# Kernel optimization log

Measured on AMD Instinct MI355X. Metric: run time of the kernel, lower is better.

Reference implementation:

```python
import jax, jax.numpy as jnp
import numpy as np


def setup_inputs() -> dict:
    key = jax.random.key(0)
    ks = jax.random.split(key, 8)
    b, l, d_model = 2, 2048, 1024
    d_inner, d_state, dt_rank, d_conv = 2048, 16, 64, 4
    g = lambda k, shape, s: jax.random.normal(k, shape, jnp.float32) * s
    A = jnp.broadcast_to(jnp.arange(1, d_state + 1, dtype=jnp.float32), (d_inner, d_state))
    return {
        "x": g(ks[0], (b, l, d_model), 1.0),
        "W_in": g(ks[1], (d_model, 2 * d_inner), 0.02),
        "W_conv": g(ks[2], (d_inner, 1, d_conv), 0.1),
        "b_conv": g(ks[3], (d_inner,), 0.1),
        "W_x": g(ks[4], (d_inner, dt_rank + 2 * d_state), 0.02),
        "W_dt": g(ks[5], (dt_rank, d_inner), 0.02),
        "b_dt": g(ks[6], (d_inner,), 0.1),
        "A_log": jnp.log(A),
        "D": jnp.ones((d_inner,), jnp.float32),
        "W_out": g(ks[7], (d_inner, d_model), 0.02),
    }


def _selective_scan(x, delta, A, B, C, D):
    # x, delta: (b, l, d); A: (d, n); B, C: (b, l, n); D: (d,)
    b, l, d = x.shape
    n = A.shape[1]

    def step(h, inp):
        dt, Bt, Ct, xt = inp  # (b,d), (b,n), (b,n), (b,d)
        dA = jnp.exp(dt[:, :, None] * A)                     # (b,d,n)
        h = dA * h + (dt * xt)[:, :, None] * Bt[:, None, :]  # (b,d,n)
        y = jnp.einsum('bdn,bn->bd', h, Ct)
        return h, y

    h0 = jnp.zeros((b, d, n), x.dtype)
    xs = (jnp.swapaxes(delta, 0, 1), jnp.swapaxes(B, 0, 1),
          jnp.swapaxes(C, 0, 1), jnp.swapaxes(x, 0, 1))
    _, ys = jax.lax.scan(step, h0, xs)   # ys: (l, b, d)
    return jnp.swapaxes(ys, 0, 1) + D * x


def _mamba(x, W_in, W_conv, b_conv, W_x, W_dt, b_dt, A_log, D, W_out):
    b, l, _ = x.shape
    d_inner = W_conv.shape[0]
    d_conv = W_conv.shape[2]
    dt_rank = W_dt.shape[0]
    n = A_log.shape[1]

    xr = x @ W_in                                   # (b,l,2*d_inner)
    xin, res = xr[..., :d_inner], xr[..., d_inner:]

    # depthwise causal conv1d (left pad d_conv-1 == torch pad both + trim to l)
    xc = jnp.swapaxes(xin, 1, 2)                    # (b,d_inner,l)
    xc = jax.lax.conv_general_dilated(
        xc, W_conv, window_strides=(1,), padding=[(d_conv - 1, 0)],
        feature_group_count=d_inner,
        dimension_numbers=('NCH', 'OIH', 'NCH')) + b_conv[None, :, None]
    xs = jax.nn.silu(jnp.swapaxes(xc, 1, 2))        # (b,l,d_inner)

    x_dbl = xs @ W_x                                # (b,l,dt_rank+2n)
    delta = jax.nn.softplus(x_dbl[..., :dt_rank] @ W_dt + b_dt)
    Bm = x_dbl[..., dt_rank:dt_rank + n]
    Cm = x_dbl[..., dt_rank + n:]
    A = -jnp.exp(A_log)

    y = _selective_scan(xs, delta, A, Bm, Cm, D)
    y = y * jax.nn.silu(res)
    return y @ W_out


def reference(x, W_in, W_conv, b_conv, W_x, W_dt, b_dt, A_log, D, W_out):
    return _mamba(x, W_in, W_conv, b_conv, W_x, W_dt, b_dt, A_log, D, W_out)
```

## Files before the change

kernel.cpp:

```cpp
#include <hip/hip_runtime.h>


typedef unsigned short ushort_t;
using short8 = __attribute__((ext_vector_type(8))) short;
using f32x4  = __attribute__((ext_vector_type(4))) float;
using gptr_t = const __attribute__((address_space(1))) unsigned short*;
using sptr_t = __attribute__((address_space(3))) unsigned short*;

#define NC 64
#define CL 32

__device__ inline ushort_t f2bf(float v) {
    unsigned u = __float_as_uint(v);
    unsigned r = (u + 0x7fff + ((u >> 16) & 1)) >> 16;
    return (ushort_t)r;
}
__device__ inline float bf2f(ushort_t h) { return __uint_as_float(((unsigned)h) << 16); }
__device__ inline void split2(float v, ushort_t& h, ushort_t& l) {
    h = f2bf(v);
    l = f2bf(v - bf2f(h));
}


__global__ void split_plain4(const float* __restrict__ in, ushort_t* __restrict__ h,
                             ushort_t* __restrict__ l, int n4) {
    int i = blockIdx.x * blockDim.x + threadIdx.x;
    if (i >= n4) return;
    float4 v = ((const float4*)in)[i];
    ushort4 hh, ll;
    split2(v.x, hh.x, ll.x); split2(v.y, hh.y, ll.y);
    split2(v.z, hh.z, ll.z); split2(v.w, hh.w, ll.w);
    ((ushort4*)h)[i] = hh;
    ((ushort4*)l)[i] = ll;
}

__global__ __launch_bounds__(256) void split_transpose(
    const float* __restrict__ W, ushort_t* __restrict__ Th, ushort_t* __restrict__ Tl,
    int K, int N) {
    __shared__ float tile[32][33];
    int n0 = blockIdx.x * 32, k0 = blockIdx.y * 32;
    int tx = threadIdx.x & 31, ty = threadIdx.x >> 5;
    #pragma unroll
    for (int j = 0; j < 4; ++j) {
        int k = ty + j * 8;
        tile[k][tx] = (n0 + tx < N) ? W[(size_t)(k0 + k) * N + n0 + tx] : 0.f;
    }
    __syncthreads();
    #pragma unroll
    for (int j = 0; j < 4; ++j) {
        int nrow = ty + j * 8;
        float v = tile[tx][nrow];
        ushort_t h, l;
        split2(v, h, l);
        size_t o = (size_t)(n0 + nrow) * K + k0 + tx;
        Th[o] = h; Tl[o] = l;
    }
}

__global__ __launch_bounds__(256) void gemm_mfma3(
    const ushort_t* __restrict__ Ah, const ushort_t* __restrict__ Al,
    const ushort_t* __restrict__ Bh, const ushort_t* __restrict__ Bl,
    float* __restrict__ C, int M, int N, int K) {
    __shared__ ushort_t sAh[4096], sAl[4096], sBh[4096], sBl[4096];
    const int tid  = threadIdx.x;
    const int wid  = tid >> 6;
    const int lane = tid & 63;
    const int bm = blockIdx.y * 128;
    const int bn = blockIdx.x * 128;
    const int wr = wid >> 1, wc = wid & 1;

    f32x4 acc[4][4];
    #pragma unroll
    for (int i = 0; i < 4; ++i)
        #pragma unroll
        for (int j = 0; j < 4; ++j) acc[i][j] = (f32x4){0.f, 0.f, 0.f, 0.f};

    for (int k0 = 0; k0 < K; k0 += 32) {
        #pragma unroll
        for (int issue = 0; issue < 2; ++issue) {
            const int off = wid * 2048 + issue * 1024 + lane * 16;
            const int row = off >> 6;
            const int ce  = (off & 63) >> 1;
            const size_t ga = (size_t)(bm + row) * K + k0 + ce;
            const size_t gb = (size_t)(bn + row) * K + k0 + ce;
            const int lo = (wid * 2048 + issue * 1024) >> 1;
            __builtin_amdgcn_global_load_lds((gptr_t)(Ah + ga), (sptr_t)&sAh[lo], 16, 0, 0);
            __builtin_amdgcn_global_load_lds((gptr_t)(Al + ga), (sptr_t)&sAl[lo], 16, 0, 0);
            __builtin_amdgcn_global_load_lds((gptr_t)(Bh + gb), (sptr_t)&sBh[lo], 16, 0, 0);
            __builtin_amdgcn_global_load_lds((gptr_t)(Bl + gb), (sptr_t)&sBl[lo], 16, 0, 0);
        }
        __syncthreads();

        const int fr = lane & 15;
        const int kb = (lane >> 4) * 8;
        short8 ah[4], al[4], bh[4], bl[4];
        #pragma unroll
        for (int i = 0; i < 4; ++i) {
            const int ra = (wr * 64 + i * 16 + fr) * 32 + kb;
            ah[i] = *(const short8*)&sAh[ra];
            al[i] = *(const short8*)&sAl[ra];
            const int rb = (wc * 64 + i * 16 + fr) * 32 + kb;
            bh[i] = *(const short8*)&sBh[rb];
            bl[i] = *(const short8*)&sBl[rb];
        }
        #pragma unroll
        for (int i = 0; i < 4; ++i)
            #pragma unroll
            for (int j = 0; j < 4; ++j) {
                acc[i][j] = __builtin_amdgcn_mfma_f32_16x16x32_bf16(ah[i], bh[j], acc[i][j], 0, 0, 0);
                acc[i][j] = __builtin_amdgcn_mfma_f32_16x16x32_bf16(ah[i], bl[j], acc[i][j], 0, 0, 0);
                acc[i][j] = __builtin_amdgcn_mfma_f32_16x16x32_bf16(al[i], bh[j], acc[i][j], 0, 0, 0);
            }
        __syncthreads();
    }

    #pragma unroll
    for (int i = 0; i < 4; ++i) {
        int row = bm + wr * 64 + i * 16 + (lane >> 4) * 4;
        #pragma unroll
        for (int j = 0; j < 4; ++j) {
            int col = bn + wc * 64 + j * 16 + (lane & 15);
            float* cp = C + (size_t)row * N + col;
            #pragma unroll
            for (int r = 0; r < 4; ++r) cp[(size_t)r * N] = acc[i][j][r];
        }
    }
}

__global__ __launch_bounds__(256) void gemm_mfma3_sk(
    const ushort_t* __restrict__ Ah, const ushort_t* __restrict__ Al,
    const ushort_t* __restrict__ Bh, const ushort_t* __restrict__ Bl,
    float* __restrict__ partial, int K) {
    __shared__ ushort_t sAh[4096], sAl[4096], sBh[4096], sBl[4096];
    const int tid  = threadIdx.x;
    const int wid  = tid >> 6;
    const int lane = tid & 63;
    const int kslice = blockIdx.x;
    const int bm = blockIdx.y * 128;
    const int wr = wid >> 1, wc = wid & 1;
    const int kbeg = kslice * 256;

    f32x4 acc[4][4];
    #pragma unroll
    for (int i = 0; i < 4; ++i)
        #pragma unroll
        for (int j = 0; j < 4; ++j) acc[i][j] = (f32x4){0.f, 0.f, 0.f, 0.f};

    for (int k0 = kbeg; k0 < kbeg + 256; k0 += 32) {
        #pragma unroll
        for (int issue = 0; issue < 2; ++issue) {
            const int off = wid * 2048 + issue * 1024 + lane * 16;
            const int row = off >> 6;
            const int ce  = (off & 63) >> 1;
            const size_t ga = (size_t)(bm + row) * K + k0 + ce;
            const size_t gb = (size_t)row * K + k0 + ce;
            const int lo = (wid * 2048 + issue * 1024) >> 1;
            __builtin_amdgcn_global_load_lds((gptr_t)(Ah + ga), (sptr_t)&sAh[lo], 16, 0, 0);
            __builtin_amdgcn_global_load_lds((gptr_t)(Al + ga), (sptr_t)&sAl[lo], 16, 0, 0);
            __builtin_amdgcn_global_load_lds((gptr_t)(Bh + gb), (sptr_t)&sBh[lo], 16, 0, 0);
            __builtin_amdgcn_global_load_lds((gptr_t)(Bl + gb), (sptr_t)&sBl[lo], 16, 0, 0);
        }
        __syncthreads();

        const int fr = lane & 15;
        const int kb = (lane >> 4) * 8;
        short8 ah[4], al[4], bh[4], bl[4];
        #pragma unroll
        for (int i = 0; i < 4; ++i) {
            const int ra = (wr * 64 + i * 16 + fr) * 32 + kb;
            ah[i] = *(const short8*)&sAh[ra];
            al[i] = *(const short8*)&sAl[ra];
            const int rb = (wc * 64 + i * 16 + fr) * 32 + kb;
            bh[i] = *(const short8*)&sBh[rb];
            bl[i] = *(const short8*)&sBl[rb];
        }
        #pragma unroll
        for (int i = 0; i < 4; ++i)
            #pragma unroll
            for (int j = 0; j < 4; ++j) {
                acc[i][j] = __builtin_amdgcn_mfma_f32_16x16x32_bf16(ah[i], bh[j], acc[i][j], 0, 0, 0);
                acc[i][j] = __builtin_amdgcn_mfma_f32_16x16x32_bf16(ah[i], bl[j], acc[i][j], 0, 0, 0);
                acc[i][j] = __builtin_amdgcn_mfma_f32_16x16x32_bf16(al[i], bh[j], acc[i][j], 0, 0, 0);
            }
        __syncthreads();
    }

    float* Cp = partial + (size_t)kslice * 4096 * 128;
    #pragma unroll
    for (int i = 0; i < 4; ++i) {
        int row = bm + wr * 64 + i * 16 + (lane >> 4) * 4;
        #pragma unroll
        for (int j = 0; j < 4; ++j) {
            int col = wc * 64 + j * 16 + (lane & 15);
            float* cp = Cp + (size_t)row * 128 + col;
            #pragma unroll
            for (int r = 0; r < 4; ++r) cp[(size_t)r * 128] = acc[i][j][r];
        }
    }
}

__global__ void reduce8(const float4* __restrict__ p, float4* __restrict__ outp) {
    int i = blockIdx.x * 256 + threadIdx.x;
    float4 s = p[i];
    #pragma unroll
    for (int k = 1; k < 8; ++k) {
        float4 v = p[i + k * 131072];
        s.x += v.x; s.y += v.y; s.z += v.z; s.w += v.w;
    }
    outp[i] = s;
}

#define BM 64
#define BN 64
#define BKK 16
__global__ __launch_bounds__(256) void gemm_f32(
    const float* __restrict__ A, const float* __restrict__ B, float* __restrict__ C,
    int M, int N, int K, int lda, int ldb, int ldc,
    const float* __restrict__ bias, int epi) {
    __shared__ float As[BKK][BM];
    __shared__ float Bs[BKK][BN];
    const int bm = blockIdx.y * BM;
    const int bn = blockIdx.x * BN;
    const int tid = threadIdx.x;
    const int tx = tid & 15;
    const int ty = tid >> 4;
    const int a_row = tid >> 2;
    const int a_col = (tid & 3) * 4;
    const int b_row = tid >> 4;
    const int b_col = (tid & 15) * 4;
    const bool fullN = (bn + BN <= N);

    float acc[4][4] = {};
    for (int k0 = 0; k0 < K; k0 += BKK) {
        {
            const float* ap = A + (size_t)(bm + a_row) * lda + (k0 + a_col);
            float4 av = *(const float4*)ap;
            As[a_col + 0][a_row] = av.x; As[a_col + 1][a_row] = av.y;
            As[a_col + 2][a_row] = av.z; As[a_col + 3][a_row] = av.w;
        }
        {
            const float* bp = B + (size_t)(k0 + b_row) * ldb + (bn + b_col);
            float4 bv;
            if (fullN) bv = *(const float4*)bp;
            else {
                bv.x = bv.y = bv.z = bv.w = 0.f;
                int rem = N - (bn + b_col);
                if (rem > 0) bv.x = bp[0];
                if (rem > 1) bv.y = bp[1];
                if (rem > 2) bv.z = bp[2];
                if (rem > 3) bv.w = bp[3];
            }
            Bs[b_row][b_col + 0] = bv.x; Bs[b_row][b_col + 1] = bv.y;
            Bs[b_row][b_col + 2] = bv.z; Bs[b_row][b_col + 3] = bv.w;
        }
        __syncthreads();
        #pragma unroll
        for (int k = 0; k < BKK; ++k) {
            float a[4], b[4];
            #pragma unroll
            for (int i = 0; i < 4; ++i) a[i] = As[k][ty * 4 + i];
            #pragma unroll
            for (int j = 0; j < 4; ++j) b[j] = Bs[k][tx * 4 + j];
            #pragma unroll
            for (int i = 0; i < 4; ++i)
                #pragma unroll
                for (int j = 0; j < 4; ++j)
                    acc[i][j] = fmaf(a[i], b[j], acc[i][j]);
        }
        __syncthreads();
    }
    #pragma unroll
    for (int i = 0; i < 4; ++i) {
        int r = bm + ty * 4 + i;
        #pragma unroll
        for (int j = 0; j < 4; ++j) {
            int col = bn + tx * 4 + j;
            if (col < N) {
                float v = acc[i][j];
                if (epi == 1) {
                    v += bias[col];
                    v = (v > 20.f) ? v : log1pf(__expf(v));
                }
                C[(size_t)r * ldc + col] = v;
            }
        }
    }
}

__global__ void conv_silu_k(const float* __restrict__ xr, const float* __restrict__ Wc,
                            const float* __restrict__ bc, float* __restrict__ xs,
                            ushort_t* __restrict__ xsh, ushort_t* __restrict__ xsl,
                            int total) {
    for (int idx = blockIdx.x * blockDim.x + threadIdx.x; idx < total;
         idx += gridDim.x * blockDim.x) {
        int d = idx & 2047;
        int l = (idx >> 11) & 2047;
        int b = idx >> 22;
        float acc = bc[d];
        const float* wp = Wc + d * 4;
        #pragma unroll
        for (int k = 0; k < 4; ++k) {
            int ll = l - 3 + k;
            if (ll >= 0)
                acc = fmaf(xr[((size_t)(b * 2048 + ll) << 12) + d], wp[k], acc);
        }
        float v = acc / (1.f + __expf(-acc));
        xs[idx] = v;
        ushort_t h, lo;
        split2(v, h, lo);
        xsh[idx] = h;
        xsl[idx] = lo;
    }
}


__global__ __launch_bounds__(256) void scan_p1(
    const float* __restrict__ delta, const float* __restrict__ xs,
    const float* __restrict__ xdbl, const float* __restrict__ A_log,
    float* __restrict__ S, float* __restrict__ sumdt) {
    const int u = blockIdx.x * 256 + threadIdx.x;
    const int chunk = u >> 12;
    const int c = u & 4095;
    const int b = c >> 11, d = c & 2047;

    float a[16];
    #pragma unroll
    for (int i = 0; i < 4; ++i) {
        float4 v = ((const float4*)(A_log + d * 16))[i];
        a[4 * i + 0] = -__expf(v.x); a[4 * i + 1] = -__expf(v.y);
        a[4 * i + 2] = -__expf(v.z); a[4 * i + 3] = -__expf(v.w);
    }
    float h[16];
    #pragma unroll
    for (int n = 0; n < 16; ++n) h[n] = 0.f;
    float sdt = 0.f;

    const size_t row0 = (size_t)b * 2048 + (size_t)chunk * CL;
    const float4* xd4 = (const float4*)xdbl;
    #pragma unroll 2
    for (int t = 0; t < CL; ++t) {
        const size_t row = row0 + t;
        float dt = delta[row * 2048 + d];
        float xv = xs[row * 2048 + d];
        float4 Bv[4];
        #pragma unroll
        for (int i = 0; i < 4; ++i) Bv[i] = xd4[row * 32 + 16 + i];
        const float* Bf = (const float*)Bv;
        sdt += dt;
        float du = dt * xv;
        #pragma unroll
        for (int n = 0; n < 16; ++n) {
            float dA = __expf(dt * a[n]);
            h[n] = fmaf(dA, h[n], du * Bf[n]);
        }
    }
    float4* S4 = (float4*)(S + ((size_t)chunk * 4096 + c) * 16);
    #pragma unroll
    for (int i = 0; i < 4; ++i)
        S4[i] = make_float4(h[4 * i + 0], h[4 * i + 1], h[4 * i + 2], h[4 * i + 3]);
    sumdt[chunk * 4096 + c] = sdt;
}

__global__ __launch_bounds__(256) void scan_p2(
    float* __restrict__ S, const float* __restrict__ sumdt,
    const float* __restrict__ A_log) {
    const int idx = blockIdx.x * blockDim.x + threadIdx.x;
    const int n = idx & 15;
    const int c = (idx >> 4) & 4095;
    const int d = c & 2047;
    const float a = -__expf(A_log[d * 16 + n]);
    float h = 0.f;
    for (int k = 0; k < NC; ++k) {
        const size_t o = ((size_t)k * 4096 + c) * 16 + n;
        float carry = S[o];
        S[o] = h;
        float P = __expf(a * sumdt[k * 4096 + c]);
        h = fmaf(P, h, carry);
    }
}

__global__ __launch_bounds__(256) void scan_p3(
    const float* __restrict__ delta, const float* __restrict__ xs,
    const float* __restrict__ xdbl, const float* __restrict__ xr,
    const float* __restrict__ A_log, const float* __restrict__ Dp,
    const float* __restrict__ H0,
    ushort_t* __restrict__ yh, ushort_t* __restrict__ yl) {
    const int u = blockIdx.x * 256 + threadIdx.x;
    const int chunk = u >> 12;
    const int c = u & 4095;
    const int b = c >> 11, d = c & 2047;

    float a[16];
    #pragma unroll
    for (int i = 0; i < 4; ++i) {
        float4 v = ((const float4*)(A_log + d * 16))[i];
        a[4 * i + 0] = -__expf(v.x); a[4 * i + 1] = -__expf(v.y);
        a[4 * i + 2] = -__expf(v.z); a[4 * i + 3] = -__expf(v.w);
    }
    float h[16];
    const float4* H4 = (const float4*)(H0 + ((size_t)chunk * 4096 + c) * 16);
    #pragma unroll
    for (int i = 0; i < 4; ++i) {
        float4 v = H4[i];
        h[4 * i + 0] = v.x; h[4 * i + 1] = v.y; h[4 * i + 2] = v.z; h[4 * i + 3] = v.w;
    }
    const float Dd = Dp[d];

    const size_t row0 = (size_t)b * 2048 + (size_t)chunk * CL;
    const float4* xd4 = (const float4*)xdbl;
    #pragma unroll 2
    for (int t = 0; t < CL; ++t) {
        const size_t row = row0 + t;
        float dt = delta[row * 2048 + d];
        float xv = xs[row * 2048 + d];
        float4 BC[8];
        #pragma unroll
        for (int i = 0; i < 8; ++i) BC[i] = xd4[row * 32 + 16 + i];
        const float* Bf = (const float*)BC;
        const float* Cf = Bf + 16;
        float du = dt * xv;
        float acc = 0.f;
        #pragma unroll
        for (int n = 0; n < 16; ++n) {
            float dA = __expf(dt * a[n]);
            h[n] = fmaf(dA, h[n], du * Bf[n]);
            acc = fmaf(h[n], Cf[n], acc);
        }
        float rv = xr[(row << 12) + 2048 + d];
        float yv = fmaf(Dd, xv, acc) * (rv / (1.f + __expf(-rv)));
        ushort_t hb, lb;
        split2(yv, hb, lb);
        yh[row * 2048 + d] = hb;
        yl[row * 2048 + d] = lb;
    }
}

extern "C" void kernel_launch(void* const* d_in, const int* in_sizes, int n_in,
                              void* d_out, int out_size, void* d_ws, size_t ws_size,
                              hipStream_t stream) {
    const float* x      = (const float*)d_in[0];
    const float* W_in   = (const float*)d_in[1];
    const float* W_conv = (const float*)d_in[2];
    const float* b_conv = (const float*)d_in[3];
    const float* W_x    = (const float*)d_in[4];
    const float* W_dt   = (const float*)d_in[5];
    const float* b_dt   = (const float*)d_in[6];
    const float* A_log  = (const float*)d_in[7];
    const float* Dp     = (const float*)d_in[8];
    const float* W_out  = (const float*)d_in[9];
    float* out = (float*)d_out;

    float* ws    = (float*)d_ws;
    float* xr    = ws;
    float* xs    = xr + 16777216;
    float* xdbl  = xs + 8388608;
    float* delta = xdbl + 524288;
    float* S     = delta + 8388608;
    float* sumdt = S + 4194304;
    ushort_t* base = (ushort_t*)(sumdt + 262144);
    ushort_t* xh = base, *xl = base + 4194304;
    ushort_t* winh = base + 8388608, *winl = base + 12582912;
    ushort_t* wouth = base + 16777216, *woutl = base + 18874368;
    ushort_t* wxh = base + 20971520, *wxl = base + 21233664;
    ushort_t* xsh = base + 21495808, *xsl = base + 29884416;
    ushort_t* yh = base, *yl = base + 8388608;
    float* partial = (float*)base;

    dim3 blk(256);

    split_plain4<<<dim3(4096), blk, 0, stream>>>(x, xh, xl, 1048576);
    split_transpose<<<dim3(128, 32), blk, 0, stream>>>(W_in, winh, winl, 1024, 4096);
    split_transpose<<<dim3(32, 64), blk, 0, stream>>>(W_out, wouth, woutl, 2048, 1024);
    split_transpose<<<dim3(4, 64), blk, 0, stream>>>(W_x, wxh, wxl, 2048, 96);

    gemm_mfma3<<<dim3(32, 32), blk, 0, stream>>>(xh, xl, winh, winl, xr, 4096, 4096, 1024);
    conv_silu_k<<<dim3(4096), blk, 0, stream>>>(xr, W_conv, b_conv, xs, xsh, xsl, 8388608);
    gemm_mfma3_sk<<<dim3(8, 32), blk, 0, stream>>>(xsh, xsl, wxh, wxl, partial, 2048);
    reduce8<<<dim3(512), blk, 0, stream>>>((const float4*)partial, (float4*)xdbl);
    gemm_f32<<<dim3(32, 64), blk, 0, stream>>>(xdbl, W_dt, delta, 4096, 2048, 64,
                                               128, 2048, 2048, b_dt, 1);
    scan_p1<<<dim3(1024), blk, 0, stream>>>(delta, xs, xdbl, A_log, S, sumdt);
    scan_p2<<<dim3(256), blk, 0, stream>>>(S, sumdt, A_log);
    scan_p3<<<dim3(1024), blk, 0, stream>>>(delta, xs, xdbl, xr, A_log, Dp, S, yh, yl);
    gemm_mfma3<<<dim3(8, 32), blk, 0, stream>>>(yh, yl, wouth, woutl, out, 4096, 1024, 2048);
}
```

Measured before the change: 538.6 us.

## Move dt projection to split-bf16 MFMA, swizzle GEMM tiles, drop fp32 xs

The fp32 SIMT GEMM for the dt projection is replaced by the split-bf16 MFMA GEMM, with the softplus bias epilogue fused in. The input is split to hi/lo bf16 inside the split-K reduce kernel, and W_dt is split-transposed up front. MFMA GEMMs gain an XCD-style block swizzle, and the output GEMM uses a new 128x64 tile variant for more workgroups. The fp32 xs buffer is dropped, so the scan kernels rebuild xs from its hi/lo halves, cutting write traffic at the cost of two loads per element.

```diff
diff --git a/kernel.cpp b/kernel.cpp
--- a/kernel.cpp
+++ b/kernel.cpp
@@ -60,13 +60,24 @@
 __global__ __launch_bounds__(256) void gemm_mfma3(
     const ushort_t* __restrict__ Ah, const ushort_t* __restrict__ Al,
     const ushort_t* __restrict__ Bh, const ushort_t* __restrict__ Bl,
-    float* __restrict__ C, int M, int N, int K) {
+    float* __restrict__ C, int M, int N, int K,
+    const float* __restrict__ bias, int epi) {
     __shared__ ushort_t sAh[4096], sAl[4096], sBh[4096], sBl[4096];
     const int tid  = threadIdx.x;
     const int wid  = tid >> 6;
     const int lane = tid & 63;
-    const int bm = blockIdx.y * 128;
-    const int bn = blockIdx.x * 128;
+    int bx = blockIdx.x, by = blockIdx.y;
+    {
+        int nwg = gridDim.x * gridDim.y;
+        if ((nwg & 7) == 0) {
+            int flat = by * gridDim.x + bx;
+            int swz = (flat & 7) * (nwg >> 3) + (flat >> 3);
+            bx = swz % gridDim.x;
+            by = swz / gridDim.x;
+        }
+    }
+    const int bm = by * 128;
+    const int bn = bx * 128;
     const int wr = wid >> 1, wc = wid & 1;
 
     f32x4 acc[4][4];
@@ -120,6 +131,102 @@
         #pragma unroll
         for (int j = 0; j < 4; ++j) {
             int col = bn + wc * 64 + j * 16 + (lane & 15);
+            float* cp = C + (size_t)row * N + col;
+            #pragma unroll
+            for (int r = 0; r < 4; ++r) {
+                float v = acc[i][j][r];
+                if (epi == 1) {
+                    v += bias[col];
+                    v = (v > 20.f) ? v : log1pf(__expf(v));
+                }
+                cp[(size_t)r * N] = v;
+            }
+        }
+    }
+}
+
+__global__ __launch_bounds__(256) void gemm_mfma3_n64(
+    const ushort_t* __restrict__ Ah, const ushort_t* __restrict__ Al,
+    const ushort_t* __restrict__ Bh, const ushort_t* __restrict__ Bl,
+    float* __restrict__ C, int M, int N, int K) {
+    __shared__ ushort_t sAh[4096], sAl[4096], sBh[2048], sBl[2048];
+    const int tid  = threadIdx.x;
+    const int wid  = tid >> 6;
+    const int lane = tid & 63;
+    int bx = blockIdx.x, by = blockIdx.y;
+    {
+        int nwg = gridDim.x * gridDim.y;
+        if ((nwg & 7) == 0) {
+            int flat = by * gridDim.x + bx;
+            int swz = (flat & 7) * (nwg >> 3) + (flat >> 3);
+            bx = swz % gridDim.x;
+            by = swz / gridDim.x;
+        }
+    }
+    const int bm = by * 128;
+    const int bn = bx * 64;
+    const int wr = wid >> 1, wc = wid & 1;
+
+    f32x4 acc[4][2];
+    #pragma unroll
+    for (int i = 0; i < 4; ++i)
+        #pragma unroll
+        for (int j = 0; j < 2; ++j) acc[i][j] = (f32x4){0.f, 0.f, 0.f, 0.f};
+
+    for (int k0 = 0; k0 < K; k0 += 32) {
+        #pragma unroll
+        for (int issue = 0; issue < 2; ++issue) {
+            const int off = issue * 4096 + tid * 16;
+            const int row = off >> 6;
+            const int ce  = (off & 63) >> 1;
+            const size_t ga = (size_t)(bm + row) * K + k0 + ce;
+            const int lo = (issue * 4096 + wid * 1024) >> 1;
+            __builtin_amdgcn_global_load_lds((gptr_t)(Ah + ga), (sptr_t)&sAh[lo], 16, 0, 0);
+            __builtin_amdgcn_global_load_lds((gptr_t)(Al + ga), (sptr_t)&sAl[lo], 16, 0, 0);
+        }
+        {
+            const int off = tid * 16;
+            const int row = off >> 6;
+            const int ce  = (off & 63) >> 1;
+            const size_t gb = (size_t)(bn + row) * K + k0 + ce;
+            const int lo = (wid * 1024) >> 1;
+            __builtin_amdgcn_global_load_lds((gptr_t)(Bh + gb), (sptr_t)&sBh[lo], 16, 0, 0);
+            __builtin_amdgcn_global_load_lds((gptr_t)(Bl + gb), (sptr_t)&sBl[lo], 16, 0, 0);
+        }
+        __syncthreads();
+
+        const int fr = lane & 15;
+        const int kb = (lane >> 4) * 8;
+        short8 ah[4], al[4], bh[2], bl[2];
+        #pragma unroll
+        for (int i = 0; i < 4; ++i) {
+            const int ra = (wr * 64 + i * 16 + fr) * 32 + kb;
+            ah[i] = *(const short8*)&sAh[ra];
+            al[i] = *(const short8*)&sAl[ra];
+        }
+        #pragma unroll
+        for (int j = 0; j < 2; ++j) {
+            const int rb = (wc * 32 + j * 16 + fr) * 32 + kb;
+            bh[j] = *(const short8*)&sBh[rb];
+            bl[j] = *(const short8*)&sBl[rb];
+        }
+        #pragma unroll
+        for (int i = 0; i < 4; ++i)
+            #pragma unroll
+            for (int j = 0; j < 2; ++j) {
+                acc[i][j] = __builtin_amdgcn_mfma_f32_16x16x32_bf16(ah[i], bh[j], acc[i][j], 0, 0, 0);
+                acc[i][j] = __builtin_amdgcn_mfma_f32_16x16x32_bf16(ah[i], bl[j], acc[i][j], 0, 0, 0);
+                acc[i][j] = __builtin_amdgcn_mfma_f32_16x16x32_bf16(al[i], bh[j], acc[i][j], 0, 0, 0);
+            }
+        __syncthreads();
+    }
+
+    #pragma unroll
+    for (int i = 0; i < 4; ++i) {
+        int row = bm + wr * 64 + i * 16 + (lane >> 4) * 4;
+        #pragma unroll
+        for (int j = 0; j < 2; ++j) {
+            int col = bn + wc * 32 + j * 16 + (lane & 15);
             float* cp = C + (size_t)row * N + col;
             #pragma unroll
             for (int r = 0; r < 4; ++r) cp[(size_t)r * N] = acc[i][j][r];
@@ -199,7 +306,8 @@
     }
 }
 
-__global__ void reduce8(const float4* __restrict__ p, float4* __restrict__ outp) {
+__global__ void reduce8split(const float4* __restrict__ p, float4* __restrict__ outp,
+                             ushort_t* __restrict__ dh, ushort_t* __restrict__ dl) {
     int i = blockIdx.x * 256 + threadIdx.x;
     float4 s = p[i];
     #pragma unroll
@@ -208,87 +316,19 @@
         s.x += v.x; s.y += v.y; s.z += v.z; s.w += v.w;
     }
     outp[i] = s;
-}
-
-#define BM 64
-#define BN 64
-#define BKK 16
-__global__ __launch_bounds__(256) void gemm_f32(
-    const float* __restrict__ A, const float* __restrict__ B, float* __restrict__ C,
-    int M, int N, int K, int lda, int ldb, int ldc,
-    const float* __restrict__ bias, int epi) {
-    __shared__ float As[BKK][BM];
-    __shared__ float Bs[BKK][BN];
-    const int bm = blockIdx.y * BM;
-    const int bn = blockIdx.x * BN;
-    const int tid = threadIdx.x;
-    const int tx = tid & 15;
-    const int ty = tid >> 4;
-    const int a_row = tid >> 2;
-    const int a_col = (tid & 3) * 4;
-    const int b_row = tid >> 4;
-    const int b_col = (tid & 15) * 4;
-    const bool fullN = (bn + BN <= N);
-
-    float acc[4][4] = {};
-    for (int k0 = 0; k0 < K; k0 += BKK) {
-        {
-            const float* ap = A + (size_t)(bm + a_row) * lda + (k0 + a_col);
-            float4 av = *(const float4*)ap;
-            As[a_col + 0][a_row] = av.x; As[a_col + 1][a_row] = av.y;
-            As[a_col + 2][a_row] = av.z; As[a_col + 3][a_row] = av.w;
-        }
-        {
-            const float* bp = B + (size_t)(k0 + b_row) * ldb + (bn + b_col);
-            float4 bv;
-            if (fullN) bv = *(const float4*)bp;
-            else {
-                bv.x = bv.y = bv.z = bv.w = 0.f;
-                int rem = N - (bn + b_col);
-                if (rem > 0) bv.x = bp[0];
-                if (rem > 1) bv.y = bp[1];
-                if (rem > 2) bv.z = bp[2];
-                if (rem > 3) bv.w = bp[3];
-            }
-            Bs[b_row][b_col + 0] = bv.x; Bs[b_row][b_col + 1] = bv.y;
-            Bs[b_row][b_col + 2] = bv.z; Bs[b_row][b_col + 3] = bv.w;
-        }
-        __syncthreads();
-        #pragma unroll
-        for (int k = 0; k < BKK; ++k) {
-            float a[4], b[4];
-            #pragma unroll
-            for (int i = 0; i < 4; ++i) a[i] = As[k][ty * 4 + i];
-            #pragma unroll
-            for (int j = 0; j < 4; ++j) b[j] = Bs[k][tx * 4 + j];
-            #pragma unroll
-            for (int i = 0; i < 4; ++i)
-                #pragma unroll
-                for (int j = 0; j < 4; ++j)
-                    acc[i][j] = fmaf(a[i], b[j], acc[i][j]);
-        }
-        __syncthreads();
-    }
-    #pragma unroll
-    for (int i = 0; i < 4; ++i) {
-        int r = bm + ty * 4 + i;
-        #pragma unroll
-        for (int j = 0; j < 4; ++j) {
-            int col = bn + tx * 4 + j;
-            if (col < N) {
-                float v = acc[i][j];
-                if (epi == 1) {
-                    v += bias[col];
-                    v = (v > 20.f) ? v : log1pf(__expf(v));
-                }
-                C[(size_t)r * ldc + col] = v;
-            }
-        }
+    int c4 = i & 31;
+    if (c4 < 16) {
+        int row = i >> 5;
+        ushort4 hh, ll;
+        split2(s.x, hh.x, ll.x); split2(s.y, hh.y, ll.y);
+        split2(s.z, hh.z, ll.z); split2(s.w, hh.w, ll.w);
+        ((ushort4*)dh)[row * 16 + c4] = hh;
+        ((ushort4*)dl)[row * 16 + c4] = ll;
     }
 }
 
 __global__ void conv_silu_k(const float* __restrict__ xr, const float* __restrict__ Wc,
-                            const float* __restrict__ bc, float* __restrict__ xs,
+                            const float* __restrict__ bc,
                             ushort_t* __restrict__ xsh, ushort_t* __restrict__ xsl,
                             int total) {
     for (int idx = blockIdx.x * blockDim.x + threadIdx.x; idx < total;
@@ -305,7 +345,6 @@
                 acc = fmaf(xr[((size_t)(b * 2048 + ll) << 12) + d], wp[k], acc);
         }
         float v = acc / (1.f + __expf(-acc));
-        xs[idx] = v;
         ushort_t h, lo;
         split2(v, h, lo);
         xsh[idx] = h;
@@ -315,7 +354,8 @@
 
 
 __global__ __launch_bounds__(256) void scan_p1(
-    const float* __restrict__ delta, const float* __restrict__ xs,
+    const float* __restrict__ delta,
+    const ushort_t* __restrict__ xsh, const ushort_t* __restrict__ xsl,
     const float* __restrict__ xdbl, const float* __restrict__ A_log,
     float* __restrict__ S, float* __restrict__ sumdt) {
     const int u = blockIdx.x * 256 + threadIdx.x;
@@ -341,7 +381,7 @@
     for (int t = 0; t < CL; ++t) {
         const size_t row = row0 + t;
         float dt = delta[row * 2048 + d];
-        float xv = xs[row * 2048 + d];
+        float xv = bf2f(xsh[row * 2048 + d]) + bf2f(xsl[row * 2048 + d]);
         float4 Bv[4];
         #pragma unroll
         for (int i = 0; i < 4; ++i) Bv[i] = xd4[row * 32 + 16 + i];
@@ -380,7 +420,8 @@
 }
 
 __global__ __launch_bounds__(256) void scan_p3(
-    const float* __restrict__ delta, const float* __restrict__ xs,
+    const float* __restrict__ delta,
+    const ushort_t* __restrict__ xsh, const ushort_t* __restrict__ xsl,
     const float* __restrict__ xdbl, const float* __restrict__ xr,
     const float* __restrict__ A_log, const float* __restrict__ Dp,
     const float* __restrict__ H0,
@@ -412,7 +453,7 @@
     for (int t = 0; t < CL; ++t) {
         const size_t row = row0 + t;
         float dt = delta[row * 2048 + d];
-        float xv = xs[row * 2048 + d];
+        float xv = bf2f(xsh[row * 2048 + d]) + bf2f(xsl[row * 2048 + d]);
         float4 BC[8];
         #pragma unroll
         for (int i = 0; i < 8; ++i) BC[i] = xd4[row * 32 + 16 + i];
@@ -452,19 +493,20 @@
 
     float* ws    = (float*)d_ws;
     float* xr    = ws;
-    float* xs    = xr + 16777216;
-    float* xdbl  = xs + 8388608;
+    float* xdbl  = xr + 16777216;
     float* delta = xdbl + 524288;
     float* S     = delta + 8388608;
     float* sumdt = S + 4194304;
     ushort_t* base = (ushort_t*)(sumdt + 262144);
     ushort_t* xh = base, *xl = base + 4194304;
     ushort_t* winh = base + 8388608, *winl = base + 12582912;
+    float*    partial = (float*)base;
+    ushort_t* yh = base, *yl = base + 8388608;
     ushort_t* wouth = base + 16777216, *woutl = base + 18874368;
-    ushort_t* wxh = base + 20971520, *wxl = base + 21233664;
-    ushort_t* xsh = base + 21495808, *xsl = base + 29884416;
-    ushort_t* yh = base, *yl = base + 8388608;
-    float* partial = (float*)base;
+    ushort_t* wxh   = base + 20971520, *wxl   = base + 21233664;
+    ushort_t* wdth  = base + 21495808, *wdtl  = base + 21626880;
+    ushort_t* dAh   = base + 21757952, *dAl   = base + 22020096;
+    ushort_t* xsh   = base + 22282240, *xsl   = base + 30670848;
 
     dim3 blk(256);
 
@@ -472,15 +514,19 @@
     split_transpose<<<dim3(128, 32), blk, 0, stream>>>(W_in, winh, winl, 1024, 4096);
     split_transpose<<<dim3(32, 64), blk, 0, stream>>>(W_out, wouth, woutl, 2048, 1024);
     split_transpose<<<dim3(4, 64), blk, 0, stream>>>(W_x, wxh, wxl, 2048, 96);
-
-    gemm_mfma3<<<dim3(32, 32), blk, 0, stream>>>(xh, xl, winh, winl, xr, 4096, 4096, 1024);
-    conv_silu_k<<<dim3(4096), blk, 0, stream>>>(xr, W_conv, b_conv, xs, xsh, xsl, 8388608);
+    split_transpose<<<dim3(64, 2), blk, 0, stream>>>(W_dt, wdth, wdtl, 64, 2048);
+
+    gemm_mfma3<<<dim3(32, 32), blk, 0, stream>>>(xh, xl, winh, winl, xr,
+                                                 4096, 4096, 1024, nullptr, 0);
+    conv_silu_k<<<dim3(4096), blk, 0, stream>>>(xr, W_conv, b_conv, xsh, xsl, 8388608);
     gemm_mfma3_sk<<<dim3(8, 32), blk, 0, stream>>>(xsh, xsl, wxh, wxl, partial, 2048);
-    reduce8<<<dim3(512), blk, 0, stream>>>((const float4*)partial, (float4*)xdbl);
-    gemm_f32<<<dim3(32, 64), blk, 0, stream>>>(xdbl, W_dt, delta, 4096, 2048, 64,
-                                               128, 2048, 2048, b_dt, 1);
-    scan_p1<<<dim3(1024), blk, 0, stream>>>(delta, xs, xdbl, A_log, S, sumdt);
+    reduce8split<<<dim3(512), blk, 0, stream>>>((const float4*)partial, (float4*)xdbl,
+                                                dAh, dAl);
+    gemm_mfma3<<<dim3(16, 32), blk, 0, stream>>>(dAh, dAl, wdth, wdtl, delta,
+                                                 4096, 2048, 64, b_dt, 1);
+    scan_p1<<<dim3(1024), blk, 0, stream>>>(delta, xsh, xsl, xdbl, A_log, S, sumdt);
     scan_p2<<<dim3(256), blk, 0, stream>>>(S, sumdt, A_log);
-    scan_p3<<<dim3(1024), blk, 0, stream>>>(delta, xs, xdbl, xr, A_log, Dp, S, yh, yl);
-    gemm_mfma3<<<dim3(8, 32), blk, 0, stream>>>(yh, yl, wouth, woutl, out, 4096, 1024, 2048);
-}
+    scan_p3<<<dim3(1024), blk, 0, stream>>>(delta, xsh, xsl, xdbl, xr, A_log, Dp, S, yh, yl);
+    gemm_mfma3_n64<<<dim3(16, 32), blk, 0, stream>>>(yh, yl, wouth, woutl, out,
+                                                     4096, 1024, 2048);
+}
```

Result: no change. 541.0 us (+0.5%).
